# Kernel tuning notes

Measured on AMD Instinct MI355X. Metric: run time of the kernel, lower is better.

## Reference

```python
import jax, jax.numpy as jnp
import numpy as np

B, C, H, L = 4, 1, 1024, 8192
KD, NS = 64, 4  # kernel_dim, num_scales


def _interp_linear(x, out_len):
    """F.interpolate(mode='linear', align_corners=False) along last axis."""
    in_len = x.shape[-1]
    if out_len == in_len:
        return x
    scale = out_len / in_len
    coord = (jnp.arange(out_len, dtype=jnp.float32) + 0.5) / scale - 0.5
    coord = jnp.clip(coord, 0.0, in_len - 1)
    lo = jnp.floor(coord).astype(jnp.int32)
    hi = jnp.minimum(lo + 1, in_len - 1)
    w = coord - lo.astype(jnp.float32)
    return x[..., lo] * (1.0 - w) + x[..., hi] * w


def setup_inputs() -> dict:
    key = jax.random.key(0)
    ks = jax.random.split(key, 8)
    u = jax.random.normal(ks[0], (B, H, L), jnp.float32)
    k0 = jax.random.normal(ks[1], (C, H, KD), jnp.float32)
    k1 = jax.random.normal(ks[2], (C, H, KD), jnp.float32)
    k2 = jax.random.normal(ks[3], (C, H, KD), jnp.float32)
    k3 = jax.random.normal(ks[4], (C, H, KD), jnp.float32)
    D = jax.random.normal(ks[5], (C, H), jnp.float32)
    W = jax.random.normal(ks[6], (H, C * H), jnp.float32) / np.float32(np.sqrt(C * H))
    b = jnp.zeros((H,), jnp.float32)
    return {"u": u, "k0": k0, "k1": k1, "k2": k2, "k3": k3, "D": D, "W": W, "b": b}


def reference(u, k0, k1, k2, k3, D, W, b):
    Lq = u.shape[-1]
    kernels = [k0, k1, k2, k3]
    total = KD * 2 ** (NS - 1)  # 512
    # multi-scale kernel build: interpolate -> right-pad -> scale -> sum
    parts = []
    for i in range(NS):
        ki = _interp_linear(kernels[i], KD * 2 ** i)
        ki = jnp.pad(ki, ((0, 0), (0, 0), (0, total - KD * 2 ** i)))
        parts.append(ki * (2.0 ** (NS - i - 1)))
    k = parts[0] + parts[1] + parts[2] + parts[3]  # (C,H,512)
    # fit to sequence length L
    if k.shape[-1] > Lq:
        k = k[..., :Lq]
    elif k.shape[-1] < Lq:
        k = jnp.pad(k, ((0, 0), (0, 0), (0, Lq - k.shape[-1])))
    # detached kernel norm
    knorm = jax.lax.stop_gradient(
        jnp.linalg.norm(k, axis=-1, keepdims=True))
    k = k / knorm
    # FFT long convolution
    n = 2 * Lq
    k_f = jnp.fft.rfft(k, n=n)              # (C,H,L+1) complex
    u_f = jnp.fft.rfft(u, n=n)              # (B,H,L+1) complex
    y_f = jnp.einsum('bhl,chl->bchl', u_f, k_f)
    y = jnp.fft.irfft(y_f, n=n)[..., :Lq]   # (B,C,H,L)
    # D skip (outer product)
    y = y + jnp.einsum('bhl,ch->bchl', u, D)
    y = y.reshape(y.shape[0], C * H, Lq)    # (B,C*H,L)
    # activation (exact gelu, torch default), dropout=Identity, norm=Identity
    y = jax.nn.gelu(y, approximate=False)
    # output_linear: 1x1 conv (C*H -> H) with bias, Identity post-activation
    y = jnp.einsum('bfl,of->bol', y, W) + b[None, :, None]
    return y
```

## Files before the change

### kernel.cpp

```cpp
#include <hip/hip_runtime.h>
#include <cstdint>
#include <cstddef>

#define HH 1024
#define LL 8192
#define NB 4
#define KD 64
#define KLEN 512

typedef float v4f  __attribute__((ext_vector_type(4)));
typedef float v16f __attribute__((ext_vector_type(16)));
typedef short v8s  __attribute__((ext_vector_type(8)));

__device__ __forceinline__ unsigned short f2bf(float f) {
  union { float f; unsigned int u; } x; x.f = f;
  unsigned int r = x.u + 0x7fffu + ((x.u >> 16) & 1u);
  return (unsigned short)(r >> 16);
}

__device__ __forceinline__ float bfbits2f(unsigned int hi16) {
  union { unsigned int u; float f; } x; x.u = hi16;
  return x.f;
}

__device__ __forceinline__ float gelu_f(float y) {
  float x = y * 0.70710678118654752f;
  float ax = fabsf(x);
  float t = __builtin_amdgcn_rcpf(fmaf(0.3275911f, ax, 1.0f));
  float p = t * fmaf(t, fmaf(t, fmaf(t, fmaf(t, 1.061405429f, -1.453152027f),
                                     1.421413741f), -0.284496736f), 0.254829592f);
  float e = __expf(-x * x);
  float erfax = fmaf(-p, e, 1.0f);
  float er = copysignf(erfax, x);
  return 0.5f * y * (1.0f + er);
}

__global__ __launch_bounds__(512) void build_k_kernel(
    const float* __restrict__ k0, const float* __restrict__ k1,
    const float* __restrict__ k2, const float* __restrict__ k3,
    float* __restrict__ kout) {
  __shared__ float lk[4][KD];
  __shared__ float red[512];
  const int h = blockIdx.x;
  const int t = threadIdx.x;
  if (t < 256) {
    int i = t >> 6, j = t & 63;
    const float* src = (i == 0) ? k0 : (i == 1) ? k1 : (i == 2) ? k2 : k3;
    lk[i][j] = src[h * KD + j];
  }
  __syncthreads();
  float kt = 0.f;
#pragma unroll
  for (int i = 0; i < 4; i++) {
    int len = KD << i;
    if (t < len) {
      float inv = 1.0f / (float)(1 << i);
      float c = ((float)t + 0.5f) * inv - 0.5f;
      c = fminf(fmaxf(c, 0.0f), 63.0f);
      int lo = (int)floorf(c);
      int hi = min(lo + 1, 63);
      float w = c - (float)lo;
      float v = lk[i][lo] * (1.0f - w) + lk[i][hi] * w;
      kt += v * (float)(1 << (3 - i));
    }
  }
  red[t] = kt * kt;
  __syncthreads();
  for (int s = 256; s > 0; s >>= 1) {
    if (t < s) red[t] += red[t + s];
    __syncthreads();
  }
  float norm = sqrtf(red[0]);
  kout[h * KLEN + t] = kt / norm;
}

__global__ void w2bf_kernel(const float* __restrict__ W,
                            unsigned short* __restrict__ Wb, int n) {
  int i = blockIdx.x * blockDim.x + threadIdx.x;
  if (i < n) Wb[i] = f2bf(W[i]);
}

__device__ __forceinline__ int suswz(int b) { return b ^ (((b >> 7) & 3) << 4); }

__global__ __launch_bounds__(256) void conv_kernel(
    const float* __restrict__ u, const float* __restrict__ kk,
    const float* __restrict__ D, unsigned short* __restrict__ g) {
  __shared__ __align__(16) unsigned short Apk[34 * 512];
  __shared__ __align__(16) unsigned short su[512 + LL];
  __shared__ __align__(16) float skk[KLEN];

  const int h = blockIdx.x;
  const int tid = threadIdx.x;
  const int w = tid >> 6;
  const int ln = tid & 63;
  const int n = ln & 31;
  const int q = ln >> 5;
  char* sub = (char*)su;

  if (tid < 128) *(float4*)(skk + tid * 4) = *(const float4*)(kk + (size_t)h * KLEN + tid * 4);
  __syncthreads();

#pragma unroll 4
  for (int e = 0; e < 68; ++e) {
    int idx = e * 256 + tid;
    int s = idx >> 9;
    int lane = (idx >> 3) & 63;
    int j = idx & 7;
    int m = lane & 31, q2 = lane >> 5;
    int c = ((s & 1) << 4) + (q2 << 3) + j;
    int t = ((s >> 1) << 5) + m - c;
    Apk[idx] = (t >= 0 && t < KLEN) ? f2bf(skk[t]) : (unsigned short)0;
  }
  __syncthreads();

  v8s af[34];
#pragma unroll
  for (int s = 0; s < 34; ++s)
    af[s] = *(const v8s*)(Apk + (s << 9) + (ln << 3));

  const float Dh = D[h];
  const int bbyte0 = 1024 + 64 * (w * 64 + n) + 16 * q;

  for (int b = 0; b < NB; ++b) {
    __syncthreads();
    const float* __restrict__ urow = u + ((size_t)b * HH + h) * LL;
    if (tid < 64) {
      uint4 z; z.x = 0; z.y = 0; z.z = 0; z.w = 0;
      *(uint4*)(sub + suswz(tid * 16)) = z;
    }
#pragma unroll
    for (int r = 0; r < 8; ++r) {
      int i = r * 1024 + tid * 4;
      float4 v = *(const float4*)(urow + i);
      uint2 p;
      p.x = (unsigned)f2bf(v.x) | ((unsigned)f2bf(v.y) << 16);
      p.y = (unsigned)f2bf(v.z) | ((unsigned)f2bf(v.w) << 16);
      *(uint2*)(sub + suswz(1024 + 2 * i)) = p;
    }
    __syncthreads();

    v16f acc0, acc1;
#pragma unroll
    for (int r = 0; r < 16; ++r) { acc0[r] = 0.f; acc1[r] = 0.f; }

#pragma unroll
    for (int s = 0; s < 34; ++s) {
      const int offb = ((s & 1) << 5) - ((s >> 1) << 6);
      const char* pb = sub + suswz(bbyte0 + offb);
      v8s b0 = *(const v8s*)(pb);
      v8s b1 = *(const v8s*)(pb + 2048);
      acc0 = __builtin_amdgcn_mfma_f32_32x32x16_bf16(af[s], b0, acc0, 0, 0, 0);
      acc1 = __builtin_amdgcn_mfma_f32_32x32x16_bf16(af[s], b1, acc1, 0, 0, 0);
    }

    unsigned short* grow = g + ((size_t)b * HH + h) * LL;
#pragma unroll
    for (int t = 0; t < 2; ++t) {
      const int i0 = w * 64 + t * 32;
#pragma unroll
      for (int rg = 0; rg < 4; ++rg) {
        const int l = 32 * (i0 + n) + 8 * rg + 4 * q;
        uint2 up2 = *(const uint2*)(sub + suswz(1024 + 2 * l));
        float uf[4];
        uf[0] = bfbits2f(up2.x << 16);
        uf[1] = bfbits2f(up2.x & 0xffff0000u);
        uf[2] = bfbits2f(up2.y << 16);
        uf[3] = bfbits2f(up2.y & 0xffff0000u);
        unsigned short hb[4];
#pragma unroll
        for (int rr = 0; rr < 4; ++rr) {
          float y = (t ? acc1[rg * 4 + rr] : acc0[rg * 4 + rr]) + Dh * uf[rr];
          hb[rr] = f2bf(gelu_f(y));
        }
        uint2 p;
        p.x = (unsigned)hb[0] | ((unsigned)hb[1] << 16);
        p.y = (unsigned)hb[2] | ((unsigned)hb[3] << 16);
        *(uint2*)(grow + l) = p;
      }
    }
  }
}

__device__ __forceinline__ void gll16(const void* g, void* l) {
  __builtin_amdgcn_global_load_lds(
      (const __attribute__((address_space(1))) unsigned int*)g,
      (__attribute__((address_space(3))) unsigned int*)l, 16, 0, 0);
}

__global__ __launch_bounds__(256) void gemm_kernel(
    const unsigned short* __restrict__ A,
    const unsigned short* __restrict__ G,
    const float* __restrict__ bias, float* __restrict__ out) {
  __shared__ __align__(16) unsigned short sA[2][4096];
  __shared__ __align__(16) unsigned int   sB[2][2048];
  const int tid = threadIdx.x;
  const int wv = tid >> 6, ln = tid & 63;

  const int bid0 = blockIdx.x;
  const int swz = (bid0 & 7) * 256 + (bid0 >> 3);
  const int mt = swz & 7, nt = swz >> 3;
  const int o0 = mt * 128;
  const int bb = nt >> 6;
  const int l0 = (nt & 63) * 128;
  const int m16 = ln & 15, q4 = ln >> 4;
  const int wm = wv & 1, wn = wv >> 1;

  v4f acc[4][4];
#pragma unroll
  for (int i = 0; i < 4; i++)
#pragma unroll
    for (int j = 0; j < 4; j++) {
      v4f z = {0.f, 0.f, 0.f, 0.f};
      acc[i][j] = z;
    }

  const unsigned short* gA[2];
  int lA[2];
  {
    const int cc = (((ln & 3) ^ ((ln >> 3) & 3)) << 3);
#pragma unroll
    for (int qq = 0; qq < 2; qq++) {
      const int c = wv * 2 + qq;
      const int rr = c * 16 + (ln >> 2);
      gA[qq] = A + (size_t)(o0 + rr) * HH + cc;
      lA[qq] = c * 512;
    }
  }

  const int pr = tid >> 4, seg = tid & 15;
  const unsigned short* gB0 = G + ((size_t)bb * HH + 2 * pr) * LL + l0 + seg * 8;
  const unsigned short* gB1 = gB0 + LL;
  int wby[8];
#pragma unroll
  for (int e = 0; e < 8; e++) {
    int l = seg * 8 + e;
    int byi = (pr >> 2) * 2048 + l * 16 + (pr & 3) * 4;
    wby[e] = byi ^ (((l >> 3) & 7) << 4);
  }

  int aby[4], bby[4];
#pragma unroll
  for (int i = 0; i < 4; i++) {
    int row = wm * 64 + i * 16 + m16;
    aby[i] = (row * 64 + q4 * 16) ^ (((m16 >> 1) & 3) << 4);
  }
#pragma unroll
  for (int j = 0; j < 4; j++) {
    int l = wn * 64 + j * 16 + m16;
    bby[j] = (q4 * 2048 + l * 16) ^ (((l >> 3) & 7) << 4);
  }

  auto stageA = [&](int buf, int kbase) {
#pragma unroll
    for (int qq = 0; qq < 2; qq++) gll16(gA[qq] + kbase, &sA[buf][lA[qq]]);
  };
  auto packB = [&](int buf, const uint4& r0, const uint4& r1) {
    union { uint4 u; unsigned short s[8]; } ua, ub; ua.u = r0; ub.u = r1;
    char* base = (char*)sB[buf];
#pragma unroll
    for (int e = 0; e < 8; e++) {
      unsigned v = (unsigned)ua.s[e] | ((unsigned)ub.s[e] << 16);
      *(unsigned*)(base + wby[e]) = v;
    }
  };

  uint4 p0, p1, c0, c1;
  stageA(0, 0);
  __builtin_amdgcn_sched_barrier(0);
  p0 = *(const uint4*)(gB0); p1 = *(const uint4*)(gB1);
  __builtin_amdgcn_sched_barrier(0);
  c0 = *(const uint4*)(gB0 + (size_t)32 * LL);
  c1 = *(const uint4*)(gB1 + (size_t)32 * LL);
  __builtin_amdgcn_sched_barrier(0);
  packB(0, p0, p1);
  asm volatile("s_waitcnt vmcnt(2) lgkmcnt(0)" ::: "memory");
  __builtin_amdgcn_s_barrier();

  for (int kk = 0; kk < 30; ++kk) {
    const int p = kk & 1;
    v8s af[4], bf4[4];
    const char* ab = (const char*)sA[p];
    const char* bbc = (const char*)sB[p];
#pragma unroll
    for (int i = 0; i < 4; i++) af[i] = *(const v8s*)(ab + aby[i]);
#pragma unroll
    for (int j = 0; j < 4; j++) bf4[j] = *(const v8s*)(bbc + bby[j]);
    stageA(p ^ 1, (kk + 1) * 32);
    __builtin_amdgcn_sched_barrier(0);
    uint4 n0 = *(const uint4*)(gB0 + (size_t)(kk + 2) * 32 * LL);
    uint4 n1 = *(const uint4*)(gB1 + (size_t)(kk + 2) * 32 * LL);
    asm volatile("s_waitcnt lgkmcnt(0)" ::: "memory");
    __builtin_amdgcn_sched_barrier(0);
    __builtin_amdgcn_s_setprio(1);
#pragma unroll
    for (int i = 0; i < 4; i++)
#pragma unroll
      for (int j = 0; j < 4; j++)
        acc[i][j] = __builtin_amdgcn_mfma_f32_16x16x32_bf16(af[i], bf4[j], acc[i][j], 0, 0, 0);
    __builtin_amdgcn_s_setprio(0);
    asm volatile("s_waitcnt vmcnt(4)" ::: "memory");
    packB(p ^ 1, c0, c1);
    c0 = n0; c1 = n1;
    asm volatile("s_waitcnt vmcnt(2) lgkmcnt(0)" ::: "memory");
    __builtin_amdgcn_s_barrier();
  }

  {
    v8s af[4], bf4[4];
    const char* ab = (const char*)sA[0];
    const char* bbc = (const char*)sB[0];
#pragma unroll
    for (int i = 0; i < 4; i++) af[i] = *(const v8s*)(ab + aby[i]);
#pragma unroll
    for (int j = 0; j < 4; j++) bf4[j] = *(const v8s*)(bbc + bby[j]);
    stageA(1, 31 * 32);
    asm volatile("s_waitcnt lgkmcnt(0)" ::: "memory");
    __builtin_amdgcn_sched_barrier(0);
    __builtin_amdgcn_s_setprio(1);
#pragma unroll
    for (int i = 0; i < 4; i++)
#pragma unroll
      for (int j = 0; j < 4; j++)
        acc[i][j] = __builtin_amdgcn_mfma_f32_16x16x32_bf16(af[i], bf4[j], acc[i][j], 0, 0, 0);
    __builtin_amdgcn_s_setprio(0);
    asm volatile("s_waitcnt vmcnt(2)" ::: "memory");
    packB(1, c0, c1);
    asm volatile("s_waitcnt vmcnt(0) lgkmcnt(0)" ::: "memory");
    __builtin_amdgcn_s_barrier();
  }
  {
    v8s af[4], bf4[4];
    const char* ab = (const char*)sA[1];
    const char* bbc = (const char*)sB[1];
#pragma unroll
    for (int i = 0; i < 4; i++) af[i] = *(const v8s*)(ab + aby[i]);
#pragma unroll
    for (int j = 0; j < 4; j++) bf4[j] = *(const v8s*)(bbc + bby[j]);
    asm volatile("s_waitcnt lgkmcnt(0)" ::: "memory");
    __builtin_amdgcn_sched_barrier(0);
    __builtin_amdgcn_s_setprio(1);
#pragma unroll
    for (int i = 0; i < 4; i++)
#pragma unroll
      for (int j = 0; j < 4; j++)
        acc[i][j] = __builtin_amdgcn_mfma_f32_16x16x32_bf16(af[i], bf4[j], acc[i][j], 0, 0, 0);
    __builtin_amdgcn_s_setprio(0);
  }

#pragma unroll
  for (int i = 0; i < 4; i++) {
    const int ob = o0 + wm * 64 + i * 16 + q4 * 4;
#pragma unroll
    for (int j = 0; j < 4; j++) {
      const int l = l0 + wn * 64 + j * 16 + m16;
#pragma unroll
      for (int r = 0; r < 4; r++) {
        const int o = ob + r;
        out[((size_t)bb * HH + o) * LL + l] = acc[i][j][r] + bias[o];
      }
    }
  }
}

extern "C" void kernel_launch(void* const* d_in, const int* in_sizes, int n_in,
                              void* d_out, int out_size, void* d_ws, size_t ws_size,
                              hipStream_t stream) {
  const float* u   = (const float*)d_in[0];
  const float* k0  = (const float*)d_in[1];
  const float* k1  = (const float*)d_in[2];
  const float* k2  = (const float*)d_in[3];
  const float* k3  = (const float*)d_in[4];
  const float* D   = (const float*)d_in[5];
  const float* W   = (const float*)d_in[6];
  const float* bia = (const float*)d_in[7];
  float* out = (float*)d_out;

  char* ws = (char*)d_ws;
  unsigned short* g  = (unsigned short*)ws;
  float* kws         = (float*)(ws + (size_t)67108864);
  unsigned short* Wb = (unsigned short*)(ws + (size_t)69206016);

  build_k_kernel<<<HH, 512, 0, stream>>>(k0, k1, k2, k3, kws);
  w2bf_kernel<<<(HH * HH + 255) / 256, 256, 0, stream>>>(W, Wb, HH * HH);
  conv_kernel<<<HH, 256, 0, stream>>>(u, kws, D, g);
  gemm_kernel<<<8 * 256, 256, 0, stream>>>(Wb, g, bia, out);
}
```

Measured before the change: 397.2 us.

## Split conv kernel across sequence halves and read Toeplitz operand from LDS

The conv kernel now launches two blocks per channel, each handling half of the sequence with a 512-sample halo loaded from the preceding half. Each wave computes one 32x32 output tile instead of two, and the Toeplitz A fragments are read from LDS inside the MFMA loop instead of being held in 34 registers. This is meant to raise the block count and occupancy by cutting LDS and register use per block. In exchange, the kernel-matrix build is repeated in both blocks and LDS reads per MFMA increase.

```diff
diff --git a/kernel.cpp b/kernel.cpp
--- a/kernel.cpp
+++ b/kernel.cpp
@@ -7,6 +7,7 @@
 #define NB 4
 #define KD 64
 #define KLEN 512
+#define LHALF 4096
 
 typedef float v4f  __attribute__((ext_vector_type(4)));
 typedef float v16f __attribute__((ext_vector_type(16)));
@@ -86,10 +87,13 @@
     const float* __restrict__ u, const float* __restrict__ kk,
     const float* __restrict__ D, unsigned short* __restrict__ g) {
   __shared__ __align__(16) unsigned short Apk[34 * 512];
-  __shared__ __align__(16) unsigned short su[512 + LL];
+  __shared__ __align__(16) unsigned short su[512 + LHALF];
   __shared__ __align__(16) float skk[KLEN];
 
-  const int h = blockIdx.x;
+  const int bid = blockIdx.x;
+  const int h = bid >> 1;
+  const int half = bid & 1;
+  const int l0 = half * LHALF;
   const int tid = threadIdx.x;
   const int w = tid >> 6;
   const int ln = tid & 63;
@@ -111,27 +115,29 @@
     int t = ((s >> 1) << 5) + m - c;
     Apk[idx] = (t >= 0 && t < KLEN) ? f2bf(skk[t]) : (unsigned short)0;
   }
-  __syncthreads();
-
-  v8s af[34];
-#pragma unroll
-  for (int s = 0; s < 34; ++s)
-    af[s] = *(const v8s*)(Apk + (s << 9) + (ln << 3));
 
   const float Dh = D[h];
-  const int bbyte0 = 1024 + 64 * (w * 64 + n) + 16 * q;
+  const int bbyte0 = 1024 + 64 * (w * 32 + n) + 16 * q;
 
   for (int b = 0; b < NB; ++b) {
     __syncthreads();
     const float* __restrict__ urow = u + ((size_t)b * HH + h) * LL;
-    if (tid < 64) {
-      uint4 z; z.x = 0; z.y = 0; z.z = 0; z.w = 0;
-      *(uint4*)(sub + suswz(tid * 16)) = z;
-    }
-#pragma unroll
-    for (int r = 0; r < 8; ++r) {
+    if (tid < 128) {
+      int i = tid * 4;
+      uint2 p;
+      if (half == 0) {
+        p.x = 0u; p.y = 0u;
+      } else {
+        float4 v = *(const float4*)(urow + l0 - 512 + i);
+        p.x = (unsigned)f2bf(v.x) | ((unsigned)f2bf(v.y) << 16);
+        p.y = (unsigned)f2bf(v.z) | ((unsigned)f2bf(v.w) << 16);
+      }
+      *(uint2*)(sub + suswz(2 * i)) = p;
+    }
+#pragma unroll
+    for (int r = 0; r < 4; ++r) {
       int i = r * 1024 + tid * 4;
-      float4 v = *(const float4*)(urow + i);
+      float4 v = *(const float4*)(urow + l0 + i);
       uint2 p;
       p.x = (unsigned)f2bf(v.x) | ((unsigned)f2bf(v.y) << 16);
       p.y = (unsigned)f2bf(v.z) | ((unsigned)f2bf(v.w) << 16);
@@ -139,44 +145,38 @@
     }
     __syncthreads();
 
-    v16f acc0, acc1;
-#pragma unroll
-    for (int r = 0; r < 16; ++r) { acc0[r] = 0.f; acc1[r] = 0.f; }
+    v16f acc;
+#pragma unroll
+    for (int r = 0; r < 16; ++r) acc[r] = 0.f;
 
 #pragma unroll
     for (int s = 0; s < 34; ++s) {
       const int offb = ((s & 1) << 5) - ((s >> 1) << 6);
-      const char* pb = sub + suswz(bbyte0 + offb);
-      v8s b0 = *(const v8s*)(pb);
-      v8s b1 = *(const v8s*)(pb + 2048);
-      acc0 = __builtin_amdgcn_mfma_f32_32x32x16_bf16(af[s], b0, acc0, 0, 0, 0);
-      acc1 = __builtin_amdgcn_mfma_f32_32x32x16_bf16(af[s], b1, acc1, 0, 0, 0);
-    }
-
-    unsigned short* grow = g + ((size_t)b * HH + h) * LL;
-#pragma unroll
-    for (int t = 0; t < 2; ++t) {
-      const int i0 = w * 64 + t * 32;
-#pragma unroll
-      for (int rg = 0; rg < 4; ++rg) {
-        const int l = 32 * (i0 + n) + 8 * rg + 4 * q;
-        uint2 up2 = *(const uint2*)(sub + suswz(1024 + 2 * l));
-        float uf[4];
-        uf[0] = bfbits2f(up2.x << 16);
-        uf[1] = bfbits2f(up2.x & 0xffff0000u);
-        uf[2] = bfbits2f(up2.y << 16);
-        uf[3] = bfbits2f(up2.y & 0xffff0000u);
-        unsigned short hb[4];
-#pragma unroll
-        for (int rr = 0; rr < 4; ++rr) {
-          float y = (t ? acc1[rg * 4 + rr] : acc0[rg * 4 + rr]) + Dh * uf[rr];
-          hb[rr] = f2bf(gelu_f(y));
-        }
-        uint2 p;
-        p.x = (unsigned)hb[0] | ((unsigned)hb[1] << 16);
-        p.y = (unsigned)hb[2] | ((unsigned)hb[3] << 16);
-        *(uint2*)(grow + l) = p;
+      v8s af = *(const v8s*)(Apk + (s << 9) + (ln << 3));
+      v8s b0 = *(const v8s*)(sub + suswz(bbyte0 + offb));
+      acc = __builtin_amdgcn_mfma_f32_32x32x16_bf16(af, b0, acc, 0, 0, 0);
+    }
+
+    unsigned short* grow = g + ((size_t)b * HH + h) * LL + l0;
+#pragma unroll
+    for (int rg = 0; rg < 4; ++rg) {
+      const int l = 32 * (w * 32 + n) + 8 * rg + 4 * q;
+      uint2 up2 = *(const uint2*)(sub + suswz(1024 + 2 * l));
+      float uf[4];
+      uf[0] = bfbits2f(up2.x << 16);
+      uf[1] = bfbits2f(up2.x & 0xffff0000u);
+      uf[2] = bfbits2f(up2.y << 16);
+      uf[3] = bfbits2f(up2.y & 0xffff0000u);
+      unsigned short hb[4];
+#pragma unroll
+      for (int rr = 0; rr < 4; ++rr) {
+        float y = acc[rg * 4 + rr] + Dh * uf[rr];
+        hb[rr] = f2bf(gelu_f(y));
       }
+      uint2 p;
+      p.x = (unsigned)hb[0] | ((unsigned)hb[1] << 16);
+      p.y = (unsigned)hb[2] | ((unsigned)hb[3] << 16);
+      *(uint2*)(grow + l) = p;
     }
   }
 }
@@ -382,6 +382,6 @@
 
   build_k_kernel<<<HH, 512, 0, stream>>>(k0, k1, k2, k3, kws);
   w2bf_kernel<<<(HH * HH + 255) / 256, 256, 0, stream>>>(W, Wb, HH * HH);
-  conv_kernel<<<HH, 256, 0, stream>>>(u, kws, D, g);
+  conv_kernel<<<HH * 2, 256, 0, stream>>>(u, kws, D, g);
   gemm_kernel<<<8 * 256, 256, 0, stream>>>(Wb, g, bia, out);
 }
```

Measured after the change: 375.4 us. 5.5% less time.
